# Optimization experiments

Measured on AMD Instinct MI355X. Metric: run time of the kernel, lower is better.

## Reference

```python
import jax, jax.numpy as jnp
import numpy as np

V, B, S = 24, 8, 512
H1, H2 = 128, 64          # mechanism hidden sizes
SH1, SH2 = 256, 128       # structure learner hidden sizes
IH = 32                   # independence test hidden
P = V * V                 # all ordered pairs (diag unused)


def _lin(k, fi, fo):
    return jax.random.normal(k, (fi, fo), dtype=jnp.float32) / np.sqrt(fi)


def setup_inputs() -> dict:
    key = jax.random.key(0)
    ks = jax.random.split(key, 18)
    data = jax.random.normal(ks[0], (B, S, V), dtype=jnp.float32)
    # structure learner: V*V -> 256 -> 128 -> V*V
    sW1, sb1 = _lin(ks[1], V * V, SH1), jnp.zeros((SH1,), jnp.float32)
    sW2, sb2 = _lin(ks[2], SH1, SH2), jnp.zeros((SH2,), jnp.float32)
    sW3, sb3 = _lin(ks[3], SH2, V * V), jnp.zeros((V * V,), jnp.float32)
    # per-variable causal mechanisms: (V-1) -> 128 -> 64 -> 1, batched over V
    mW1 = jax.random.normal(ks[4], (V, V - 1, H1), jnp.float32) / np.sqrt(V - 1)
    mb1 = jnp.zeros((V, H1), jnp.float32)
    mW2 = jax.random.normal(ks[5], (V, H1, H2), jnp.float32) / np.sqrt(H1)
    mb2 = jnp.zeros((V, H2), jnp.float32)
    mW3 = jax.random.normal(ks[6], (V, H2, 1), jnp.float32) / np.sqrt(H2)
    mb3 = jnp.zeros((V, 1), jnp.float32)
    # per-pair independence tests: 2 -> 32 -> 1, batched over P pairs
    iW1 = jax.random.normal(ks[7], (P, 2, IH), jnp.float32) / np.sqrt(2)
    ib1 = jnp.zeros((P, IH), jnp.float32)
    iW2 = jax.random.normal(ks[8], (P, IH, 1), jnp.float32) / np.sqrt(IH)
    ib2 = jnp.zeros((P, 1), jnp.float32)
    return dict(data=data, sW1=sW1, sb1=sb1, sW2=sW2, sb2=sb2, sW3=sW3, sb3=sb3,
                mW1=mW1, mb1=mb1, mW2=mW2, mb2=mb2, mW3=mW3, mb3=mb3,
                iW1=iW1, ib1=ib1, iW2=iW2, ib2=ib2)


# constant gather index: others[v] = all variable indices except v (order preserved)
_OTHERS = np.array([[j for j in range(V) if j != v] for v in range(V)])  # [V, V-1]
_II = np.repeat(np.arange(V), V)  # pair -> i
_JJ = np.tile(np.arange(V), V)    # pair -> j


def reference(data, sW1, sb1, sW2, sb2, sW3, sb3,
              mW1, mb1, mW2, mb2, mW3, mb3,
              iW1, ib1, iW2, ib2):
    relu, sig = jax.nn.relu, jax.nn.sigmoid
    b, s, v = data.shape

    # ---- correlations (vectorized torch.corrcoef over all pairs) ----
    avg = data.mean(axis=0)                       # [S, V]
    c = avg - avg.mean(axis=0, keepdims=True)
    cov = c.T @ c                                 # [V, V]
    std = jnp.sqrt(jnp.diag(cov))
    corr = jnp.abs(cov / (std[:, None] * std[None, :]))
    corr = jnp.where(jnp.isnan(corr), 0.0, corr)
    corr = corr * (1.0 - jnp.eye(v, dtype=corr.dtype))

    # ---- structure learner (dropout in eval mode = identity) ----
    h = relu(corr.reshape(1, -1) @ sW1 + sb1)
    h = relu(h @ sW2 + sb2)
    adj = sig(h @ sW3 + sb3).reshape(v, v)
    adj = jnp.triu(adj, k=1)                      # DAG: strict upper triangle

    # ---- causal mechanisms: parent-masked other-vars -> small MLP per var ----
    parent_mask = adj > 0.5                       # parent_mask[p, child]
    x_others = data[:, :, _OTHERS]                # [B, S, V, V-1]
    pmask = parent_mask[_OTHERS, np.arange(V)[:, None]]  # [V, V-1]
    xin = x_others * pmask.astype(data.dtype)[None, None]
    hm = relu(jnp.einsum('bsvf,vfh->bsvh', xin, mW1) + mb1)
    hm = relu(jnp.einsum('bsvh,vhg->bsvg', hm, mW2) + mb2)
    pred = (jnp.einsum('bsvg,vgo->bsvo', hm, mW3) + mb3)[..., 0]  # [B, S, V]
    has_parent = parent_mask.any(axis=0)          # [V]
    predictions = jnp.where(has_parent[None, None, :], pred, data)

    # ---- independence tests: per-pair 2->32->1 MLP, mean over all samples ----
    flatd = data.reshape(b * s, v)                # [N, V]
    tin = jnp.stack([flatd[:, _II], flatd[:, _JJ]], axis=-1)  # [N, P, 2]
    tin = tin.transpose(1, 0, 2)                  # [P, N, 2]
    hi = relu(jnp.einsum('pnf,pfh->pnh', tin, iW1) + ib1[:, None, :])
    si = sig(jnp.einsum('pnh,pho->pno', hi, iW2) + ib2[:, None, :])
    ind_scores = si.mean(axis=(1, 2)).reshape(v, v)

    return adj, predictions, ind_scores
```

## Files before the change

### kernel.cpp

```cpp
#include <hip/hip_runtime.h>
#include <math.h>

#define NV 24
#define NB 8
#define NS 512
#define NTOK 4096
#define H1 128
#define H2 64
#define SH1 256
#define SH2 128
#define IH 32
#define NP 576

typedef short bf16x8 __attribute__((ext_vector_type(8)));
typedef float f32x4 __attribute__((ext_vector_type(4)));

__device__ __forceinline__ short f2bf(float f) {
    union { float f; unsigned u; } x; x.f = f;
    unsigned r = x.u + 0x7fffu + ((x.u >> 16) & 1u);
    return (short)(r >> 16);
}

__device__ __forceinline__ float blk_reduce(float x, float* red, int t) {
#pragma unroll
    for (int o = 32; o > 0; o >>= 1) x += __shfl_xor(x, o);
    if ((t & 63) == 0) red[t >> 6] = x;
    __syncthreads();
    float r = red[0] + red[1] + red[2] + red[3];
    __syncthreads();
    return r;
}


__global__ __launch_bounds__(256) void k_prep(
    const float* __restrict__ data, float* __restrict__ dataT,
    const float* __restrict__ sW1, const float* __restrict__ sW2,
    const float* __restrict__ sW3,
    float* __restrict__ sW1T, float* __restrict__ sW2T, float* __restrict__ sW3T,
    const float* __restrict__ mW1, const float* __restrict__ mW2,
    const float* __restrict__ iW1, const float* __restrict__ ib1,
    const float* __restrict__ iW2,
    float* __restrict__ scratch,
    float* __restrict__ partialS, float* __restrict__ partialG) {
    __shared__ __align__(16) char L[16900];
    const int u = blockIdx.x, t = threadIdx.x;
    if (u < 384) {
        int idx = u * 256 + t;
        int n = idx / NV, v = idx % NV;
        dataT[v * NTOK + n] = data[idx];
        return;
    }
    if (u < 446) {
        float (*T)[65] = (float (*)[65])L;
        int rb = u - 384;
        const float* src; float* dst; int R, C, ti, tj;
        if (rb < 36)      { src = sW1; dst = sW1T; R = 576; C = 256; ti = rb >> 2;        tj = rb & 3; }
        else if (rb < 44) { src = sW2; dst = sW2T; R = 256; C = 128; ti = (rb - 36) >> 1; tj = (rb - 36) & 1; }
        else              { src = sW3; dst = sW3T; R = 128; C = 576; ti = (rb - 44) / 9;  tj = (rb - 44) % 9; }
        const int col = t & 63, rq = t >> 6;
#pragma unroll
        for (int i = 0; i < 16; ++i) {
            int row = i * 4 + rq;
            T[row][col] = src[(ti * 64 + row) * C + tj * 64 + col];
        }
        __syncthreads();
#pragma unroll
        for (int i = 0; i < 16; ++i) {
            int row = i * 4 + rq;
            dst[(tj * 64 + row) * R + ti * 64 + col] = T[col][row];
        }
        return;
    }
    if (u < 574) {
        const int wb = u - 446;
        float acc = 0.f;
        const float4* srcs[5] = { (const float4*)mW1, (const float4*)mW2,
                                  (const float4*)iW1, (const float4*)ib1,
                                  (const float4*)iW2 };
        const int len4[5] = { NV * 23 * H1 / 4, NV * H1 * H2 / 4,
                              NP * 2 * IH / 4, NP * IH / 4, NP * IH / 4 };
#pragma unroll
        for (int a = 0; a < 5; ++a) {
            const float4* p = srcs[a];
            const int n4 = len4[a];
            for (int idx = wb * 256 + t; idx < n4; idx += 128 * 256) {
                float4 v = p[idx];
                acc += v.x + v.y + v.z + v.w;
            }
        }
        float* red = (float*)L;
        acc = blk_reduce(acc, red, t);
        if (t == 0) scratch[wb] = acc;
        return;
    }
    const int gb = u - 574;
    float* avgL = (float*)L;
    const int s0 = gb * 64;
    for (int idx = t; idx < 64 * NV; idx += 256) {
        float a = 0.f;
#pragma unroll
        for (int b = 0; b < NB; ++b)
            a += data[(b * NS + s0) * NV + idx];
        avgL[idx] = a * 0.125f;
    }
    __syncthreads();
    if (t < NV) {
        float s = 0.f;
        for (int ss = 0; ss < 64; ++ss) s += avgL[ss * NV + t];
        partialS[gb * NV + t] = s;
    }
    for (int p = t; p < NP; p += 256) {
        int i = p / NV, j = p % NV;
        float g = 0.f;
        for (int ss = 0; ss < 64; ++ss)
            g = fmaf(avgL[ss * NV + i], avgL[ss * NV + j], g);
        partialG[gb * NP + p] = g;
    }
}

__global__ __launch_bounds__(256) void k_adj1(
    const float* __restrict__ partialG, const float* __restrict__ partialS,
    const float* __restrict__ sW1T, const float* __restrict__ sb1,
    float* __restrict__ h1out) {
    __shared__ float corrL[NP];
    __shared__ float stdL[NV];
    __shared__ float Sv[NV];
    __shared__ float red[256];
    const int o = blockIdx.x, t = threadIdx.x;
    if (t < NV) {
        float s = 0.f;
#pragma unroll
        for (int b = 0; b < NB; ++b) s += partialS[b * NV + t];
        Sv[t] = s;
    }
    __syncthreads();
    for (int k = t; k < NP; k += 256) {
        float g = 0.f;
#pragma unroll
        for (int b = 0; b < NB; ++b) g += partialG[b * NP + k];
        int i = k / NV, j = k % NV;
        corrL[k] = g - Sv[i] * Sv[j] * (1.f / NS);
    }
    __syncthreads();
    if (t < NV) stdL[t] = sqrtf(corrL[t * (NV + 1)]);
    __syncthreads();
    for (int k = t; k < NP; k += 256) {
        int i = k / NV, j = k % NV;
        float q = fabsf(corrL[k] / (stdL[i] * stdL[j]));
        if (isnan(q)) q = 0.f;
        if (i == j) q = 0.f;
        corrL[k] = q;
    }
    __syncthreads();
    const float* w = sW1T + o * 576;
    float w0 = w[t], w1 = w[256 + t];
    float w2 = (t < 64) ? w[512 + t] : 0.f;
    float c2 = (t < 64) ? corrL[512 + t] : 0.f;
    float a = corrL[t] * w0 + corrL[256 + t] * w1 + c2 * w2;
    a = blk_reduce(a, red, t);
    if (t == 0) h1out[o] = fmaxf(a + sb1[o], 0.f);
}

__global__ __launch_bounds__(256) void k_adj2(
    const float* __restrict__ h1, const float* __restrict__ sW2T,
    const float* __restrict__ sb2, float* __restrict__ h2out) {
    __shared__ float red[256];
    const int o = blockIdx.x, t = threadIdx.x;
    float a = h1[t] * sW2T[o * 256 + t];
    a = blk_reduce(a, red, t);
    if (t == 0) h2out[o] = fmaxf(a + sb2[o], 0.f);
}

__global__ __launch_bounds__(256) void k_predind(
    const float* __restrict__ data,
    const float* __restrict__ mW1, const float* __restrict__ mb1,
    const float* __restrict__ mW2, const float* __restrict__ mb2,
    const float* __restrict__ mW3, const float* __restrict__ mb3,
    const float* __restrict__ h2, const float* __restrict__ sW3T,
    const float* __restrict__ sb3,
    float* __restrict__ out_adj, float* __restrict__ out_pred,
    const float* __restrict__ dataT,
    const float* __restrict__ iW1, const float* __restrict__ ib1,
    const float* __restrict__ iW2, const float* __restrict__ ib2,
    float* __restrict__ out_ind) {
    __shared__ __align__(16) char L[34816];
    const int bx = blockIdx.x;
    const int t = threadIdx.x;

    if (bx < 768) {
        const int v = bx % NV;
        const int chunk = bx / NV;

        float* P3 = (float*)L;
        float* maskL = (float*)L + 192;
        {
            const int r3 = t >> 3, kq3 = t & 7;
            if (r3 < NV) {
                float a = 0.f;
                if (r3 < v) {
                    const float* w = sW3T + (r3 * NV + v) * 128 + kq3 * 16;
                    const float* hp2 = h2 + kq3 * 16;
#pragma unroll
                    for (int kk = 0; kk < 16; ++kk)
                        a = fmaf(hp2[kk], w[kk], a);
                }
                P3[r3 * 8 + kq3] = a;
            }
        }
        __syncthreads();
        if (t < NV) {
            float s = 0.f;
#pragma unroll
            for (int q = 0; q < 8; ++q) s += P3[t * 8 + q];
            float sg = 1.f / (1.f + expf(-(s + sb3[t * NV + v])));
            maskL[t] = (t < v && sg > 0.5f) ? 1.f : 0.f;
        }
        __syncthreads();
        bool hp = false;
#pragma unroll
        for (int r = 0; r < NV; ++r) hp = hp || (maskL[r] > 0.5f);
        float pm_reg = 0.f;
        int src1 = 0;
        if (t < 184) {
            int k = t >> 3;
            src1 = k + (k >= v ? 1 : 0);
            pm_reg = maskL[src1];
        }
        __syncthreads();

        if (!hp) {
            if (t < 128) {
                int tok = chunk * 128 + t;
                out_pred[tok * NV + v] = data[tok * NV + v];
            }
            return;
        }
        short* Xl = (short*)L;
        short* WH = (short*)(L + 10240);
        short* W1B = WH;
        short* W2B = WH + 4096;
        short* Hl = WH;

        if (t < 128) {
            int tok = chunk * 128 + t;
            const float4* dr4 = (const float4*)(data + tok * NV);
            float d[24];
#pragma unroll
            for (int q = 0; q < 6; ++q) {
                float4 uu = dr4[q];
                d[q * 4 + 0] = uu.x; d[q * 4 + 1] = uu.y; d[q * 4 + 2] = uu.z; d[q * 4 + 3] = uu.w;
            }
            short xr[32];
#pragma unroll
            for (int j = 0; j < 23; ++j) {
                int src = j + (j >= v ? 1 : 0);
                xr[j] = f2bf(d[src]);
            }
            xr[23] = f2bf(1.0f);
#pragma unroll
            for (int j = 24; j < 32; ++j) xr[j] = 0;
            short* xp = Xl + t * 40;
#pragma unroll
            for (int q = 0; q < 4; ++q)
                *(bf16x8*)(xp + q * 8) = *(bf16x8*)(xr + q * 8);
        }
        if (t < 184) {
            int k = t >> 3, h8 = (t & 7) * 16;
            const float4* wr = (const float4*)(mW1 + (v * 23 + k) * 128 + h8);
            float wv[16];
#pragma unroll
            for (int q = 0; q < 4; ++q) {
                float4 uu = wr[q];
                wv[q * 4 + 0] = uu.x; wv[q * 4 + 1] = uu.y;
                wv[q * 4 + 2] = uu.z; wv[q * 4 + 3] = uu.w;
            }
            int kb = (k >> 3) & 3, e = k & 7;
#pragma unroll
            for (int q = 0; q < 16; ++q) {
                int h = h8 + q;
                int nt = h >> 4, nn = h & 15;
                W1B[((nt * 4 + kb) * 16 + nn) * 8 + e] = f2bf(wv[q] * pm_reg);
            }
        } else if (t < 200) {
            int h8 = (t - 184) * 8;
            const float4* br = (const float4*)(mb1 + v * 128 + h8);
            float bv[8];
#pragma unroll
            for (int q = 0; q < 2; ++q) {
                float4 uu = br[q];
                bv[q * 4 + 0] = uu.x; bv[q * 4 + 1] = uu.y;
                bv[q * 4 + 2] = uu.z; bv[q * 4 + 3] = uu.w;
            }
#pragma unroll
            for (int q = 0; q < 8; ++q) {
                int h = h8 + q;
                int nt = h >> 4, nn = h & 15;
                W1B[((nt * 4 + 2) * 16 + nn) * 8 + 7] = f2bf(bv[q]);
            }
        }
        if (t < 128) {
            int nt = t >> 4, nn = t & 15;
#pragma unroll
            for (int e = 0; e < 8; ++e)
                W1B[((nt * 4 + 3) * 16 + nn) * 8 + e] = 0;
        }
        {
            int k = t >> 1, n0 = (t & 1) * 32;
            const float4* wr = (const float4*)(mW2 + (v * 128 + k) * 64 + n0);
            float wv[32];
#pragma unroll
            for (int q = 0; q < 8; ++q) {
                float4 uu = wr[q];
                wv[q * 4 + 0] = uu.x; wv[q * 4 + 1] = uu.y;
                wv[q * 4 + 2] = uu.z; wv[q * 4 + 3] = uu.w;
            }
            int s = k >> 5, kb = (k >> 3) & 3, e = k & 7;
#pragma unroll
            for (int q = 0; q < 32; ++q) {
                int n = n0 + q;
                int nt = n >> 4, nn = n & 15;
                W2B[(((s * 4 + nt) * 4 + kb) * 16 + nn) * 8 + e] = f2bf(wv[q]);
            }
        }
        __syncthreads();

        const int lane = t & 63;
        const int wid = t >> 6;
        const int ml = lane & 15;
        const int kb = lane >> 4;
        short* Hw = Hl + wid * 2048;

        bf16x8 w1f[8], w2f[16];
#pragma unroll
        for (int nt = 0; nt < 8; ++nt)
            w1f[nt] = *(bf16x8*)(W1B + (nt * 64 + lane) * 8);
#pragma unroll
        for (int q = 0; q < 16; ++q)
            w2f[q] = *(bf16x8*)(W2B + (q * 64 + lane) * 8);

        float b2r[4], w3r[4];
#pragma unroll
        for (int nt = 0; nt < 4; ++nt) {
            b2r[nt] = mb2[v * 64 + nt * 16 + ml];
            w3r[nt] = mW3[v * 64 + nt * 16 + ml];
        }
        float b3v = mb3[v];

        __syncthreads();

#pragma unroll
        for (int mt = 0; mt < 2; ++mt) {
            int lt = wid * 32 + mt * 16 + ml;
            bf16x8 a1 = *(bf16x8*)(Xl + lt * 40 + kb * 8);
            f32x4 c1[8] = {};
#pragma unroll
            for (int nt = 0; nt < 8; ++nt)
                c1[nt] = __builtin_amdgcn_mfma_f32_16x16x32_bf16(a1, w1f[nt], c1[nt], 0, 0, 0);
#pragma unroll
            for (int nt = 0; nt < 8; ++nt) {
#pragma unroll
                for (int r = 0; r < 4; ++r) {
                    int m = kb * 4 + r;
                    int h = nt * 16 + ml;
                    int bo = (m * 256 + h * 2) ^ ((m & 7) << 4);
                    *(short*)((char*)Hw + bo) = f2bf(fmaxf(c1[nt][r], 0.f));
                }
            }
            f32x4 c2[4] = {};
#pragma unroll
            for (int s = 0; s < 4; ++s) {
                int c0 = s * 32 + kb * 8;
                int bo = (ml * 256 + c0 * 2) ^ ((ml & 7) << 4);
                bf16x8 a2 = *(bf16x8*)((char*)Hw + bo);
#pragma unroll
                for (int nt = 0; nt < 4; ++nt)
                    c2[nt] = __builtin_amdgcn_mfma_f32_16x16x32_bf16(a2, w2f[s * 4 + nt], c2[nt], 0, 0, 0);
            }
            float sacc[4] = {0.f, 0.f, 0.f, 0.f};
#pragma unroll
            for (int nt = 0; nt < 4; ++nt) {
#pragma unroll
                for (int r = 0; r < 4; ++r)
                    sacc[r] += fmaxf(c2[nt][r] + b2r[nt], 0.f) * w3r[nt];
            }
#pragma unroll
            for (int o = 1; o < 16; o <<= 1) {
#pragma unroll
                for (int r = 0; r < 4; ++r)
                    sacc[r] += __shfl_xor(sacc[r], o);
            }
            if (ml == 0) {
                int tokb = chunk * 128 + wid * 32 + mt * 16 + kb * 4;
#pragma unroll
                for (int r = 0; r < 4; ++r)
                    out_pred[(tokb + r) * NV + v] = sacc[r] + b3v;
            }
        }
    } else if (bx < 1344) {
        int p = bx - 768;
        int i = p / NV, j = p % NV;
        float* red = (float*)L;
        float* wl = (float*)L + 256;
        if (t < IH) {
            wl[t]      = iW1[p * 2 * IH + t];
            wl[32 + t] = iW1[p * 2 * IH + IH + t];
            wl[64 + t] = ib1[p * IH + t];
            wl[96 + t] = iW2[p * IH + t];
        }
        __syncthreads();
        float b2v = ib2[p];
        const float* di_p = dataT + i * NTOK;
        const float* dj_p = dataT + j * NTOK;
        float di[16], dj[16], s[16];
#pragma unroll
        for (int q = 0; q < 16; ++q) {
            di[q] = di_p[q * 256 + t];
            dj[q] = dj_p[q * 256 + t];
            s[q] = b2v;
        }
#pragma unroll 4
        for (int h = 0; h < IH; ++h) {
            float w0 = wl[h], w1 = wl[32 + h], bb = wl[64 + h], w2 = wl[96 + h];
#pragma unroll
            for (int q = 0; q < 16; ++q) {
                float a = fmaf(di[q], w0, fmaf(dj[q], w1, bb));
                a = fmaxf(a, 0.f);
                s[q] = fmaf(a, w2, s[q]);
            }
        }
        float acc = 0.f;
#pragma unroll
        for (int q = 0; q < 16; ++q) acc += 1.f / (1.f + expf(-s[q]));
        __syncthreads();
        red[t] = acc;
        __syncthreads();
        for (int st = 128; st > 0; st >>= 1) {
            if (t < st) red[t] += red[t + st];
            __syncthreads();
        }
        if (t == 0) out_ind[p] = red[0] * (1.f / NTOK);
    } else {
        float* red = (float*)L;
        const int oo = bx - 1344;
        float a = (t < SH2) ? h2[t] * sW3T[oo * 128 + t] : 0.f;
        a = blk_reduce(a, red, t);
        if (t == 0) {
            float sg = 1.f / (1.f + expf(-(a + sb3[oo])));
            int i = oo / NV, j = oo % NV;
            out_adj[oo] = (j > i) ? sg : 0.f;
        }
    }
}

extern "C" void kernel_launch(void* const* d_in, const int* in_sizes, int n_in,
                              void* d_out, int out_size, void* d_ws, size_t ws_size,
                              hipStream_t stream) {
    const float* data = (const float*)d_in[0];
    const float* sW1 = (const float*)d_in[1];
    const float* sb1 = (const float*)d_in[2];
    const float* sW2 = (const float*)d_in[3];
    const float* sb2 = (const float*)d_in[4];
    const float* sW3 = (const float*)d_in[5];
    const float* sb3 = (const float*)d_in[6];
    const float* mW1 = (const float*)d_in[7];
    const float* mb1 = (const float*)d_in[8];
    const float* mW2 = (const float*)d_in[9];
    const float* mb2 = (const float*)d_in[10];
    const float* mW3 = (const float*)d_in[11];
    const float* mb3 = (const float*)d_in[12];
    const float* iW1 = (const float*)d_in[13];
    const float* ib1 = (const float*)d_in[14];
    const float* iW2 = (const float*)d_in[15];
    const float* ib2 = (const float*)d_in[16];

    float* out = (float*)d_out;
    float* ws = (float*)d_ws;
    float* ws_h1 = ws + 576;
    float* ws_h2 = ws + 832;
    float* ws_scratch = ws + 960;
    float* ws_pS = ws + 1088;
    float* ws_pG = ws + 1280;
    float* ws_dataT = ws + 8192;
    float* ws_sW1T = ws + 106496;
    float* ws_sW2T = ws + 253952;
    float* ws_sW3T = ws + 286720;

    k_prep<<<dim3(582), dim3(256), 0, stream>>>(data, ws_dataT, sW1, sW2, sW3,
                                                ws_sW1T, ws_sW2T, ws_sW3T,
                                                mW1, mW2, iW1, ib1, iW2,
                                                ws_scratch, ws_pS, ws_pG);
    k_adj1<<<dim3(SH1), dim3(256), 0, stream>>>(ws_pG, ws_pS, ws_sW1T, sb1, ws_h1);
    k_adj2<<<dim3(SH2), dim3(256), 0, stream>>>(ws_h1, ws_sW2T, sb2, ws_h2);
    k_predind<<<dim3(768 + NP + NP), dim3(256), 0, stream>>>(
        data, mW1, mb1, mW2, mb2, mW3, mb3, ws_h2, ws_sW3T, sb3,
        out, out + NP, ws_dataT, iW1, ib1, iW2, ib2, out + NP + NTOK * NV);
}
```

Before: 42.40 us.

## Fuse second structure layer and adjacency output into predind, tile data transpose

Removes the separate k_adj2 launch: each mechanism block now recomputes the 128-wide second structure-learner layer from h1 in shared memory. Adjacency outputs are written by the chunk-0 mechanism blocks instead of 576 extra blocks. The data transpose now runs in 16 blocks through a padded shared tile instead of 384 blocks with scattered writes. The cost is redundant h2 computation in every mechanism block (768 blocks each reading 128KB of sW2T, mostly from cache), traded for one fewer kernel launch and fewer blocks.

```diff
diff --git a/kernel.cpp b/kernel.cpp
--- a/kernel.cpp
+++ b/kernel.cpp
@@ -39,20 +39,28 @@
     float* __restrict__ sW1T, float* __restrict__ sW2T, float* __restrict__ sW3T,
     const float* __restrict__ mW1, const float* __restrict__ mW2,
     const float* __restrict__ iW1, const float* __restrict__ ib1,
-    const float* __restrict__ iW2,
+    const float* __restrict__ iW2, const float* __restrict__ ib2,
     float* __restrict__ scratch,
     float* __restrict__ partialS, float* __restrict__ partialG) {
-    __shared__ __align__(16) char L[16900];
+    __shared__ __align__(16) char L[25600];
     const int u = blockIdx.x, t = threadIdx.x;
-    if (u < 384) {
-        int idx = u * 256 + t;
-        int n = idx / NV, v = idx % NV;
-        dataT[v * NTOK + n] = data[idx];
+    if (u < 16) {
+        float* T = (float*)L;
+        const int n0 = u * 256;
+#pragma unroll
+        for (int it = 0; it < 24; ++it) {
+            int idx = it * 256 + t;
+            T[(idx / 24) * 25 + (idx % 24)] = data[n0 * 24 + idx];
+        }
+        __syncthreads();
+#pragma unroll
+        for (int v = 0; v < 24; ++v)
+            dataT[v * NTOK + n0 + t] = T[t * 25 + v];
         return;
     }
-    if (u < 446) {
+    if (u < 78) {
         float (*T)[65] = (float (*)[65])L;
-        int rb = u - 384;
+        int rb = u - 16;
         const float* src; float* dst; int R, C, ti, tj;
         if (rb < 36)      { src = sW1; dst = sW1T; R = 576; C = 256; ti = rb >> 2;        tj = rb & 3; }
         else if (rb < 44) { src = sW2; dst = sW2T; R = 256; C = 128; ti = (rb - 36) >> 1; tj = (rb - 36) & 1; }
@@ -71,16 +79,17 @@
         }
         return;
     }
-    if (u < 574) {
-        const int wb = u - 446;
+    if (u < 206) {
+        const int wb = u - 78;
         float acc = 0.f;
-        const float4* srcs[5] = { (const float4*)mW1, (const float4*)mW2,
+        const float4* srcs[6] = { (const float4*)mW1, (const float4*)mW2,
                                   (const float4*)iW1, (const float4*)ib1,
-                                  (const float4*)iW2 };
-        const int len4[5] = { NV * 23 * H1 / 4, NV * H1 * H2 / 4,
-                              NP * 2 * IH / 4, NP * IH / 4, NP * IH / 4 };
-#pragma unroll
-        for (int a = 0; a < 5; ++a) {
+                                  (const float4*)iW2, (const float4*)ib2 };
+        const int len4[6] = { NV * 23 * H1 / 4, NV * H1 * H2 / 4,
+                              NP * 2 * IH / 4, NP * IH / 4, NP * IH / 4,
+                              NP / 4 };
+#pragma unroll
+        for (int a = 0; a < 6; ++a) {
             const float4* p = srcs[a];
             const int n4 = len4[a];
             for (int idx = wb * 256 + t; idx < n4; idx += 128 * 256) {
@@ -93,7 +102,7 @@
         if (t == 0) scratch[wb] = acc;
         return;
     }
-    const int gb = u - 574;
+    const int gb = u - 206;
     float* avgL = (float*)L;
     const int s0 = gb * 64;
     for (int idx = t; idx < 64 * NV; idx += 256) {
@@ -161,22 +170,13 @@
     if (t == 0) h1out[o] = fmaxf(a + sb1[o], 0.f);
 }
 
-__global__ __launch_bounds__(256) void k_adj2(
-    const float* __restrict__ h1, const float* __restrict__ sW2T,
-    const float* __restrict__ sb2, float* __restrict__ h2out) {
-    __shared__ float red[256];
-    const int o = blockIdx.x, t = threadIdx.x;
-    float a = h1[t] * sW2T[o * 256 + t];
-    a = blk_reduce(a, red, t);
-    if (t == 0) h2out[o] = fmaxf(a + sb2[o], 0.f);
-}
-
 __global__ __launch_bounds__(256) void k_predind(
     const float* __restrict__ data,
     const float* __restrict__ mW1, const float* __restrict__ mb1,
     const float* __restrict__ mW2, const float* __restrict__ mb2,
     const float* __restrict__ mW3, const float* __restrict__ mb3,
-    const float* __restrict__ h2, const float* __restrict__ sW3T,
+    const float* __restrict__ h1, const float* __restrict__ sW2T,
+    const float* __restrict__ sb2, const float* __restrict__ sW3T,
     const float* __restrict__ sb3,
     float* __restrict__ out_adj, float* __restrict__ out_pred,
     const float* __restrict__ dataT,
@@ -191,15 +191,34 @@
         const int v = bx % NV;
         const int chunk = bx / NV;
 
-        float* P3 = (float*)L;
-        float* maskL = (float*)L + 192;
+        float* h1L  = (float*)L;
+        float* h2L  = (float*)L + 256;
+        float* P3   = (float*)L + 384;
+        float* maskL = (float*)L + 576;
+
+        h1L[t] = h1[t];
+        __syncthreads();
+        if (t < SH2) {
+            const float4* wr = (const float4*)(sW2T + t * 256);
+            float a = sb2[t];
+#pragma unroll
+            for (int q = 0; q < 64; ++q) {
+                float4 w = wr[q];
+                a = fmaf(h1L[q * 4 + 0], w.x, a);
+                a = fmaf(h1L[q * 4 + 1], w.y, a);
+                a = fmaf(h1L[q * 4 + 2], w.z, a);
+                a = fmaf(h1L[q * 4 + 3], w.w, a);
+            }
+            h2L[t] = fmaxf(a, 0.f);
+        }
+        __syncthreads();
         {
             const int r3 = t >> 3, kq3 = t & 7;
             if (r3 < NV) {
                 float a = 0.f;
                 if (r3 < v) {
                     const float* w = sW3T + (r3 * NV + v) * 128 + kq3 * 16;
-                    const float* hp2 = h2 + kq3 * 16;
+                    const float* hp2 = h2L + kq3 * 16;
 #pragma unroll
                     for (int kk = 0; kk < 16; ++kk)
                         a = fmaf(hp2[kk], w[kk], a);
@@ -214,16 +233,17 @@
             for (int q = 0; q < 8; ++q) s += P3[t * 8 + q];
             float sg = 1.f / (1.f + expf(-(s + sb3[t * NV + v])));
             maskL[t] = (t < v && sg > 0.5f) ? 1.f : 0.f;
+            if (chunk == 0)
+                out_adj[t * NV + v] = (t < v) ? sg : 0.f;
         }
         __syncthreads();
         bool hp = false;
 #pragma unroll
         for (int r = 0; r < NV; ++r) hp = hp || (maskL[r] > 0.5f);
         float pm_reg = 0.f;
-        int src1 = 0;
         if (t < 184) {
             int k = t >> 3;
-            src1 = k + (k >= v ? 1 : 0);
+            int src1 = k + (k >= v ? 1 : 0);
             pm_reg = maskL[src1];
         }
         __syncthreads();
@@ -396,7 +416,7 @@
                     out_pred[(tokb + r) * NV + v] = sacc[r] + b3v;
             }
         }
-    } else if (bx < 1344) {
+    } else {
         int p = bx - 768;
         int i = p / NV, j = p % NV;
         float* red = (float*)L;
@@ -439,16 +459,6 @@
             __syncthreads();
         }
         if (t == 0) out_ind[p] = red[0] * (1.f / NTOK);
-    } else {
-        float* red = (float*)L;
-        const int oo = bx - 1344;
-        float a = (t < SH2) ? h2[t] * sW3T[oo * 128 + t] : 0.f;
-        a = blk_reduce(a, red, t);
-        if (t == 0) {
-            float sg = 1.f / (1.f + expf(-(a + sb3[oo])));
-            int i = oo / NV, j = oo % NV;
-            out_adj[oo] = (j > i) ? sg : 0.f;
-        }
     }
 }
 
@@ -476,7 +486,6 @@
     float* out = (float*)d_out;
     float* ws = (float*)d_ws;
     float* ws_h1 = ws + 576;
-    float* ws_h2 = ws + 832;
     float* ws_scratch = ws + 960;
     float* ws_pS = ws + 1088;
     float* ws_pG = ws + 1280;
@@ -485,13 +494,12 @@
     float* ws_sW2T = ws + 253952;
     float* ws_sW3T = ws + 286720;
 
-    k_prep<<<dim3(582), dim3(256), 0, stream>>>(data, ws_dataT, sW1, sW2, sW3,
+    k_prep<<<dim3(214), dim3(256), 0, stream>>>(data, ws_dataT, sW1, sW2, sW3,
                                                 ws_sW1T, ws_sW2T, ws_sW3T,
-                                                mW1, mW2, iW1, ib1, iW2,
+                                                mW1, mW2, iW1, ib1, iW2, ib2,
                                                 ws_scratch, ws_pS, ws_pG);
     k_adj1<<<dim3(SH1), dim3(256), 0, stream>>>(ws_pG, ws_pS, ws_sW1T, sb1, ws_h1);
-    k_adj2<<<dim3(SH2), dim3(256), 0, stream>>>(ws_h1, ws_sW2T, sb2, ws_h2);
-    k_predind<<<dim3(768 + NP + NP), dim3(256), 0, stream>>>(
-        data, mW1, mb1, mW2, mb2, mW3, mb3, ws_h2, ws_sW3T, sb3,
+    k_predind<<<dim3(768 + NP), dim3(256), 0, stream>>>(
+        data, mW1, mb1, mW2, mb2, mW3, mb3, ws_h1, ws_sW2T, sb2, ws_sW3T, sb3,
         out, out + NP, ws_dataT, iW1, ib1, iW2, ib2, out + NP + NTOK * NV);
 }
```

Result: slower. 63.09 us (+48.8%).
